# Kernel optimization log

Hardware: AMD Instinct MI355X
Metric: run time of the kernel (lower is better)

The kernel has to match this reference:

```python
import jax, jax.numpy as jnp
import numpy as np

B, N, C, D = 64, 1024, 128, 64

def setup_inputs() -> dict:
    key = jax.random.key(0)
    ks = jax.random.split(key, 7)
    # kaiming_normal_ on weights (fan_in = C), default zero-ish biases kept as Linear default uniform; use small uniform
    std = float(np.sqrt(2.0 / C))
    bb = float(1.0 / np.sqrt(C))
    return {
        "x": jax.random.normal(ks[0], (B, N, C), jnp.float32),
        "Wq": jax.random.normal(ks[1], (C, D), jnp.float32) * std,
        "bq": jax.random.uniform(ks[2], (D,), jnp.float32, -bb, bb),
        "Wk": jax.random.normal(ks[3], (C, D), jnp.float32) * std,
        "bk": jax.random.uniform(ks[4], (D,), jnp.float32, -bb, bb),
        "Wv": jax.random.normal(ks[5], (C, D), jnp.float32) * std,
        "bv": jax.random.uniform(ks[6], (D,), jnp.float32, -bb, bb),
    }

def reference(x, Wq, bq, Wk, bk, Wv, bv):
    q = jax.nn.relu(jnp.einsum('bnc,cd->bnd', x, Wq) + bq)  # [B,N,D]
    k = jax.nn.relu(jnp.einsum('bnc,cd->bnd', x, Wk) + bk)
    v = jax.nn.relu(jnp.einsum('bnc,cd->bnd', x, Wv) + bv)
    scores = jnp.einsum('bnd,bmd->bnm', q, k) / jnp.sqrt(jnp.asarray(D, q.dtype))
    attn = jax.nn.softmax(scores, axis=-1)
    out = jnp.einsum('bnm,bmd->bnd', attn, v)
    return out + q
```

## Files before the change

### kernel.cpp

```cpp
#include <hip/hip_runtime.h>
#include <hip/hip_bf16.h>


#define Bsz 64
#define Nsz 1024
#define Csz 128
#define Dsz 64

typedef __attribute__((ext_vector_type(8))) short short8;
typedef __attribute__((ext_vector_type(4))) float f32x4;

__device__ __forceinline__ unsigned short f2bf(float f) {
    union { float f; unsigned u; } v; v.f = f;
    unsigned r = v.u + 0x7FFF + ((v.u >> 16) & 1);
    return (unsigned short)(r >> 16);
}
__device__ __forceinline__ float bf2f(unsigned short h) {
    union { unsigned u; float f; } v; v.u = ((unsigned)h) << 16;
    return v.f;
}
__device__ __forceinline__ unsigned pack_bf16rn(float lo, float hi) {
    unsigned ulo = __float_as_uint(lo) + 0x8000u;
    unsigned uhi = __float_as_uint(hi) + 0x8000u;
    return __builtin_amdgcn_perm(uhi, ulo, 0x07060302u);
}

#define SCq (0.125f * 1.44269504f)
#define INV_SC (1.0f / (0.125f * 1.44269504f))

__global__ __launch_bounds__(256) void wprep_kernel(
    const float* __restrict__ Wq, const float* __restrict__ Wk,
    const float* __restrict__ Wv, unsigned short* __restrict__ wfrag)
{
    int t = blockIdx.x * 256 + threadIdx.x;
    int lane = t & 63, ksi = (t >> 6) & 3, dt = t >> 8;
    int l16 = lane & 15, quad = lane >> 4;
    int d = dt * 16 + l16;
    int c0 = ksi * 32 + quad * 8;
    short8 h8, l8, k8, v8;
    #pragma unroll
    for (int j = 0; j < 8; j++) {
        float w = Wq[(c0 + j) * Dsz + d];
        unsigned short h = f2bf(w);
        h8[j] = (short)h;
        l8[j] = (short)f2bf(w - bf2f(h));
        k8[j] = (short)f2bf(Wk[(c0 + j) * Dsz + d]);
        v8[j] = (short)f2bf(Wv[(c0 + j) * Dsz + d]);
    }
    int idx = (dt * 4 + ksi) * 64 + lane;
    ((short8*)wfrag)[0 * 1024 + idx] = h8;
    ((short8*)wfrag)[1 * 1024 + idx] = l8;
    ((short8*)wfrag)[2 * 1024 + idx] = k8;
    ((short8*)wfrag)[3 * 1024 + idx] = v8;
}

__global__ __launch_bounds__(256) void qkv_kernel(
    const float* __restrict__ x, const unsigned short* __restrict__ wfrag,
    const float* __restrict__ bq, const float* __restrict__ bk,
    const float* __restrict__ bv,
    unsigned short* __restrict__ qs, unsigned short* __restrict__ ks2,
    unsigned short* __restrict__ vt2)
{
    __shared__ short xh[8192];
    __shared__ short xl[8192];
    const int t    = threadIdx.x;
    const int lane = t & 63;
    const int l16  = lane & 15, quad = lane >> 4;
    const int dt   = t >> 6;
    const long rowbase = (long)blockIdx.x * 64;
    const int d = dt * 16 + l16;

    short8 wqh[4], wql[4], wkf[4], wvf[4];
    #pragma unroll
    for (int ksi = 0; ksi < 4; ksi++) {
        int idx = (dt * 4 + ksi) * 64 + lane;
        wqh[ksi] = ((const short8*)wfrag)[0 * 1024 + idx];
        wql[ksi] = ((const short8*)wfrag)[1 * 1024 + idx];
        wkf[ksi] = ((const short8*)wfrag)[2 * 1024 + idx];
        wvf[ksi] = ((const short8*)wfrag)[3 * 1024 + idx];
    }

    {
        const int row = t & 63;
        const float* xrow = x + (rowbase + row) * Csz;
        #pragma unroll
        for (int p = 0; p < 4; p++) {
            int cb = (t >> 6) + p * 4;
            float4 a = *(const float4*)(xrow + cb * 8);
            float4 bb = *(const float4*)(xrow + cb * 8 + 4);
            float f[8] = {a.x, a.y, a.z, a.w, bb.x, bb.y, bb.z, bb.w};
            short8 hi, lo;
            #pragma unroll
            for (int i = 0; i < 8; i++) {
                unsigned short h = f2bf(f[i]);
                hi[i] = (short)h;
                lo[i] = (short)f2bf(f[i] - bf2f(h));
            }
            int unit = ((row >> 4) * 4 + (cb >> 2)) * 64 + ((row & 15) | ((cb & 3) << 4));
            *(short8*)&xh[unit * 8] = hi;
            *(short8*)&xl[unit * 8] = lo;
        }
    }
    __syncthreads();

    f32x4 aq[4], ak[4], av[4];
    #pragma unroll
    for (int i = 0; i < 4; i++) {
        aq[i] = (f32x4){0.f, 0.f, 0.f, 0.f};
        ak[i] = (f32x4){0.f, 0.f, 0.f, 0.f};
        av[i] = (f32x4){0.f, 0.f, 0.f, 0.f};
    }
    #pragma unroll
    for (int ksi = 0; ksi < 4; ksi++) {
        #pragma unroll
        for (int rt = 0; rt < 4; rt++) {
            short8 ah = *(const short8*)&xh[((rt * 4 + ksi) * 64 + lane) * 8];
            short8 al = *(const short8*)&xl[((rt * 4 + ksi) * 64 + lane) * 8];
            aq[rt] = __builtin_amdgcn_mfma_f32_16x16x32_bf16(ah, wqh[ksi], aq[rt], 0, 0, 0);
            aq[rt] = __builtin_amdgcn_mfma_f32_16x16x32_bf16(al, wqh[ksi], aq[rt], 0, 0, 0);
            aq[rt] = __builtin_amdgcn_mfma_f32_16x16x32_bf16(ah, wql[ksi], aq[rt], 0, 0, 0);
            ak[rt] = __builtin_amdgcn_mfma_f32_16x16x32_bf16(ah, wkf[ksi], ak[rt], 0, 0, 0);
            av[rt] = __builtin_amdgcn_mfma_f32_16x16x32_bf16(ah, wvf[ksi], av[rt], 0, 0, 0);
        }
    }

    const float bqd = bq[d], bkd = bk[d], bvd = bv[d];
    const long b  = rowbase >> 10;
    const int  kt = (int)((rowbase >> 6) & 15);

    const int half  = dt >> 1;
    const int quadk = ((dt & 1) << 1) | (l16 >> 3);
    const int jk    = l16 & 7;
    unsigned short* kbase = ks2 + ((((long)(b * 16 + kt) * 4) * 2 + half) * 64) * 8;

    float vv[4][4];
    #pragma unroll
    for (int rt = 0; rt < 4; rt++) {
        #pragma unroll
        for (int r = 0; r < 4; r++) {
            long n = rowbase + rt * 16 + quad * 4 + r;
            float q = fmaxf(aq[rt][r] + bqd, 0.f);
            float k = fmaxf(ak[rt][r] + bkd, 0.f);
            vv[r][rt] = fmaxf(av[rt][r] + bvd, 0.f);
            qs[n * Dsz + d] = f2bf(q * SCq);
            kbase[((long)rt * 2 * 64 + quadk * 16 + quad * 4 + r) * 8 + jk] = f2bf(k);
        }
    }
    const int ck = quad >> 1;
    const int quadp = (quad & 1) * 2;
    long vidx = (((long)(b * 16 + kt) * 4 + dt) * 2 + ck) * 64 + quadp * 16 + l16;
    uint4 o0 = make_uint4(pack_bf16rn(vv[0][0], vv[0][1]), pack_bf16rn(vv[0][2], vv[0][3]),
                          pack_bf16rn(vv[1][0], vv[1][1]), pack_bf16rn(vv[1][2], vv[1][3]));
    uint4 o1 = make_uint4(pack_bf16rn(vv[2][0], vv[2][1]), pack_bf16rn(vv[2][2], vv[2][3]),
                          pack_bf16rn(vv[3][0], vv[3][1]), pack_bf16rn(vv[3][2], vv[3][3]));
    ((uint4*)vt2)[vidx]      = o0;
    ((uint4*)vt2)[vidx + 16] = o1;
}

__global__ __launch_bounds__(256) void attn_kernel(
    const unsigned short* __restrict__ qs,
    const unsigned short* __restrict__ ks2,
    const unsigned short* __restrict__ vt2,
    float* __restrict__ out)
{
    __shared__ short Pl[4][32][72];

    const int t    = threadIdx.x;
    const int wave = t >> 6;
    const int lane = t & 63;
    const int l16  = lane & 15;
    const int quad = lane >> 4;
    const int b    = blockIdx.x & 63;
    const int qh   = blockIdx.x >> 6;
    const int qbase = qh * 128 + wave * 32;

    const short8* ks8 = (const short8*)ks2 + (long)b * (16 * 4 * 2 * 64);
    const short8* vt8 = (const short8*)vt2 + (long)b * (16 * 4 * 2 * 64);

    short8 aq[2][2];
    #pragma unroll
    for (int s = 0; s < 2; s++) {
        const unsigned short* qp = qs + ((long)b * Nsz + qbase + s * 16 + l16) * Dsz + quad * 8;
        aq[s][0] = *(const short8*)(qp);
        aq[s][1] = *(const short8*)(qp + 32);
    }

    f32x4 O[2][4];
    float lsum[2][4];
    #pragma unroll
    for (int s = 0; s < 2; s++)
        #pragma unroll
        for (int i = 0; i < 4; i++) { O[s][i] = (f32x4){0.f,0.f,0.f,0.f}; lsum[s][i] = 0.f; }

    short8 kf[4][2];
    #pragma unroll
    for (int kb = 0; kb < 4; kb++) {
        kf[kb][0] = ks8[(kb * 2 + 0) * 64 + lane];
        kf[kb][1] = ks8[(kb * 2 + 1) * 64 + lane];
    }

    for (int kt = 0; kt < 16; kt++) {
        short8 bvf[2][4];
        #pragma unroll
        for (int cb = 0; cb < 4; cb++) {
            bvf[0][cb] = vt8[((long)kt * 8 + cb * 2 + 0) * 64 + lane];
            bvf[1][cb] = vt8[((long)kt * 8 + cb * 2 + 1) * 64 + lane];
        }

        f32x4 sc[2][4];
        #pragma unroll
        for (int s = 0; s < 2; s++) {
            #pragma unroll
            for (int kb = 0; kb < 4; kb++) {
                f32x4 z = (f32x4){0.f, 0.f, 0.f, 0.f};
                z = __builtin_amdgcn_mfma_f32_16x16x32_bf16(aq[s][0], kf[kb][0], z, 0, 0, 0);
                z = __builtin_amdgcn_mfma_f32_16x16x32_bf16(aq[s][1], kf[kb][1], z, 0, 0, 0);
                sc[s][kb] = z;
            }
        }

        short8 kf2[4][2];
        {
            int ktn = (kt + 1) & 15;
            #pragma unroll
            for (int kb = 0; kb < 4; kb++) {
                kf2[kb][0] = ks8[((long)ktn * 8 + kb * 2 + 0) * 64 + lane];
                kf2[kb][1] = ks8[((long)ktn * 8 + kb * 2 + 1) * 64 + lane];
            }
        }

        #pragma unroll
        for (int s = 0; s < 2; s++) {
            #pragma unroll
            for (int r = 0; r < 4; r++) {
                float p0 = __builtin_amdgcn_exp2f(sc[s][0][r]);
                float p1 = __builtin_amdgcn_exp2f(sc[s][1][r]);
                float p2 = __builtin_amdgcn_exp2f(sc[s][2][r]);
                float p3 = __builtin_amdgcn_exp2f(sc[s][3][r]);
                lsum[s][r] += (p0 + p1) + (p2 + p3);
                *(uint2*)&Pl[wave][s * 16 + quad * 4 + r][l16 * 4] =
                    make_uint2(pack_bf16rn(p0, p1), pack_bf16rn(p2, p3));
            }
        }

        #pragma unroll
        for (int ck = 0; ck < 2; ck++) {
            #pragma unroll
            for (int s = 0; s < 2; s++) {
                short8 ap = *(const short8*)&Pl[wave][s * 16 + l16][ck * 32 + quad * 8];
                #pragma unroll
                for (int cb = 0; cb < 4; cb++) {
                    O[s][cb] = __builtin_amdgcn_mfma_f32_16x16x32_bf16(ap, bvf[ck][cb], O[s][cb], 0, 0, 0);
                }
            }
        }

        #pragma unroll
        for (int kb = 0; kb < 4; kb++) { kf[kb][0] = kf2[kb][0]; kf[kb][1] = kf2[kb][1]; }
    }

    #pragma unroll
    for (int s = 0; s < 2; s++)
        #pragma unroll
        for (int r = 0; r < 4; r++)
            #pragma unroll
            for (int off = 1; off < 16; off <<= 1)
                lsum[s][r] += __shfl_xor(lsum[s][r], off);

    #pragma unroll
    for (int s = 0; s < 2; s++) {
        #pragma unroll
        for (int r = 0; r < 4; r++) {
            float rl = 1.0f / lsum[s][r];
            long nrow = (long)b * Nsz + qbase + s * 16 + quad * 4 + r;
            #pragma unroll
            for (int cb = 0; cb < 4; cb++) {
                int d = cb * 16 + l16;
                float qv = bf2f(qs[nrow * Dsz + d]) * INV_SC;
                out[nrow * Dsz + d] = O[s][cb][r] * rl + qv;
            }
        }
    }
}

extern "C" void kernel_launch(void* const* d_in, const int* in_sizes, int n_in,
                              void* d_out, int out_size, void* d_ws, size_t ws_size,
                              hipStream_t stream) {
    const float* x  = (const float*)d_in[0];
    const float* Wq = (const float*)d_in[1];
    const float* bq = (const float*)d_in[2];
    const float* Wk = (const float*)d_in[3];
    const float* bk = (const float*)d_in[4];
    const float* Wv = (const float*)d_in[5];
    const float* bv = (const float*)d_in[6];
    float* out = (float*)d_out;

    char* ws = (char*)d_ws;
    unsigned short* qsc   = (unsigned short*)ws;
    unsigned short* ks2   = (unsigned short*)(ws + 0x1000000);
    unsigned short* vt2   = (unsigned short*)(ws + 0x2000000);
    unsigned short* wfrag = (unsigned short*)(ws + 0x3000000);

    wprep_kernel<<<dim3(4), dim3(256), 0, stream>>>(Wq, Wk, Wv, wfrag);
    qkv_kernel<<<dim3(1024), dim3(256), 0, stream>>>(
        x, wfrag, bq, bk, bv, qsc, ks2, vt2);
    attn_kernel<<<dim3(512), dim3(256), 0, stream>>>(
        qsc, ks2, vt2, out);
}
```

Before: 120.7 us.

## Fuse QKV projection into attention kernel, recomputing K/V per block in LDS

Merges the projection and attention kernels into one launch. Each block computes its own Q tile into shared memory and recomputes K and V for every key tile of its batch on the fly. This removes the global write and re-read of the bf16 Q/K/V intermediates and one launch. In exchange, the K/V projection work and x reads are duplicated across the 8 query blocks of each batch, and extra block-wide barriers are added per key tile.

```diff
diff --git a/kernel.cpp b/kernel.cpp
--- a/kernel.cpp
+++ b/kernel.cpp
@@ -54,21 +54,25 @@
     ((short8*)wfrag)[3 * 1024 + idx] = v8;
 }
 
-__global__ __launch_bounds__(256) void qkv_kernel(
+__global__ __launch_bounds__(256, 2) void fused_kernel(
     const float* __restrict__ x, const unsigned short* __restrict__ wfrag,
     const float* __restrict__ bq, const float* __restrict__ bk,
-    const float* __restrict__ bv,
-    unsigned short* __restrict__ qs, unsigned short* __restrict__ ks2,
-    unsigned short* __restrict__ vt2)
+    const float* __restrict__ bv, float* __restrict__ out)
 {
-    __shared__ short xh[8192];
-    __shared__ short xl[8192];
+    __shared__ short Xs[8192];
+    __shared__ short KVb[2][4096];
+    __shared__ short Qs[128][72];
+    __shared__ short Pl[4][32][72];
+
     const int t    = threadIdx.x;
     const int lane = t & 63;
-    const int l16  = lane & 15, quad = lane >> 4;
-    const int dt   = t >> 6;
-    const long rowbase = (long)blockIdx.x * 64;
-    const int d = dt * 16 + l16;
+    const int l16  = lane & 15;
+    const int quad = lane >> 4;
+    const int wave = t >> 6;
+    const int dt   = wave;
+    const int b    = blockIdx.x & 63;
+    const int qh   = blockIdx.x >> 6;
+    const int d    = dt * 16 + l16;
 
     short8 wqh[4], wql[4], wkf[4], wvf[4];
     #pragma unroll
@@ -79,134 +83,138 @@
         wkf[ksi] = ((const short8*)wfrag)[2 * 1024 + idx];
         wvf[ksi] = ((const short8*)wfrag)[3 * 1024 + idx];
     }
-
-    {
-        const int row = t & 63;
-        const float* xrow = x + (rowbase + row) * Csz;
-        #pragma unroll
-        for (int p = 0; p < 4; p++) {
-            int cb = (t >> 6) + p * 4;
-            float4 a = *(const float4*)(xrow + cb * 8);
-            float4 bb = *(const float4*)(xrow + cb * 8 + 4);
-            float f[8] = {a.x, a.y, a.z, a.w, bb.x, bb.y, bb.z, bb.w};
-            short8 hi, lo;
-            #pragma unroll
-            for (int i = 0; i < 8; i++) {
-                unsigned short h = f2bf(f[i]);
-                hi[i] = (short)h;
-                lo[i] = (short)f2bf(f[i] - bf2f(h));
-            }
-            int unit = ((row >> 4) * 4 + (cb >> 2)) * 64 + ((row & 15) | ((cb & 3) << 4));
-            *(short8*)&xh[unit * 8] = hi;
-            *(short8*)&xl[unit * 8] = lo;
-        }
-    }
-    __syncthreads();
-
-    f32x4 aq[4], ak[4], av[4];
-    #pragma unroll
-    for (int i = 0; i < 4; i++) {
-        aq[i] = (f32x4){0.f, 0.f, 0.f, 0.f};
-        ak[i] = (f32x4){0.f, 0.f, 0.f, 0.f};
-        av[i] = (f32x4){0.f, 0.f, 0.f, 0.f};
-    }
-    #pragma unroll
-    for (int ksi = 0; ksi < 4; ksi++) {
-        #pragma unroll
-        for (int rt = 0; rt < 4; rt++) {
-            short8 ah = *(const short8*)&xh[((rt * 4 + ksi) * 64 + lane) * 8];
-            short8 al = *(const short8*)&xl[((rt * 4 + ksi) * 64 + lane) * 8];
-            aq[rt] = __builtin_amdgcn_mfma_f32_16x16x32_bf16(ah, wqh[ksi], aq[rt], 0, 0, 0);
-            aq[rt] = __builtin_amdgcn_mfma_f32_16x16x32_bf16(al, wqh[ksi], aq[rt], 0, 0, 0);
-            aq[rt] = __builtin_amdgcn_mfma_f32_16x16x32_bf16(ah, wql[ksi], aq[rt], 0, 0, 0);
-            ak[rt] = __builtin_amdgcn_mfma_f32_16x16x32_bf16(ah, wkf[ksi], ak[rt], 0, 0, 0);
-            av[rt] = __builtin_amdgcn_mfma_f32_16x16x32_bf16(ah, wvf[ksi], av[rt], 0, 0, 0);
-        }
-    }
-
     const float bqd = bq[d], bkd = bk[d], bvd = bv[d];
-    const long b  = rowbase >> 10;
-    const int  kt = (int)((rowbase >> 6) & 15);
+
+    #pragma unroll 1
+    for (int h64 = 0; h64 < 2; h64++) {
+        const long rowbase = (long)b * Nsz + qh * 128 + h64 * 64;
+        {
+            const int row = t & 63;
+            const float* xrow = x + (rowbase + row) * Csz;
+            short* xl = &KVb[0][0];
+            #pragma unroll
+            for (int p = 0; p < 4; p++) {
+                int cb = (t >> 6) + p * 4;
+                float4 a  = *(const float4*)(xrow + cb * 8);
+                float4 b2 = *(const float4*)(xrow + cb * 8 + 4);
+                float f[8] = {a.x, a.y, a.z, a.w, b2.x, b2.y, b2.z, b2.w};
+                short8 hi, lo;
+                #pragma unroll
+                for (int i = 0; i < 8; i++) {
+                    unsigned short h = f2bf(f[i]);
+                    hi[i] = (short)h;
+                    lo[i] = (short)f2bf(f[i] - bf2f(h));
+                }
+                int unit = ((row >> 4) * 4 + (cb >> 2)) * 64 + ((row & 15) | ((cb & 3) << 4));
+                *(short8*)&Xs[unit * 8] = hi;
+                *(short8*)&xl[unit * 8] = lo;
+            }
+        }
+        __syncthreads();
+        f32x4 aqc[4];
+        #pragma unroll
+        for (int i = 0; i < 4; i++) aqc[i] = (f32x4){0.f, 0.f, 0.f, 0.f};
+        #pragma unroll
+        for (int ksi = 0; ksi < 4; ksi++) {
+            #pragma unroll
+            for (int rt = 0; rt < 4; rt++) {
+                short8 ah = *(const short8*)&Xs[((rt * 4 + ksi) * 64 + lane) * 8];
+                short8 al = *(const short8*)&KVb[0][((rt * 4 + ksi) * 64 + lane) * 8];
+                aqc[rt] = __builtin_amdgcn_mfma_f32_16x16x32_bf16(ah, wqh[ksi], aqc[rt], 0, 0, 0);
+                aqc[rt] = __builtin_amdgcn_mfma_f32_16x16x32_bf16(al, wqh[ksi], aqc[rt], 0, 0, 0);
+                aqc[rt] = __builtin_amdgcn_mfma_f32_16x16x32_bf16(ah, wql[ksi], aqc[rt], 0, 0, 0);
+            }
+        }
+        #pragma unroll
+        for (int rt = 0; rt < 4; rt++)
+            #pragma unroll
+            for (int r = 0; r < 4; r++) {
+                float q = fmaxf(aqc[rt][r] + bqd, 0.f);
+                Qs[h64 * 64 + rt * 16 + quad * 4 + r][d] = f2bf(q * SCq);
+            }
+        __syncthreads();
+    }
+
+    short8 aq[2][2];
+    #pragma unroll
+    for (int s = 0; s < 2; s++) {
+        aq[s][0] = *(const short8*)&Qs[wave * 32 + s * 16 + l16][quad * 8];
+        aq[s][1] = *(const short8*)&Qs[wave * 32 + s * 16 + l16][32 + quad * 8];
+    }
+
+    f32x4 O[2][4];
+    float lsum[2][4];
+    #pragma unroll
+    for (int s = 0; s < 2; s++)
+        #pragma unroll
+        for (int i = 0; i < 4; i++) { O[s][i] = (f32x4){0.f,0.f,0.f,0.f}; lsum[s][i] = 0.f; }
 
     const int half  = dt >> 1;
     const int quadk = ((dt & 1) << 1) | (l16 >> 3);
     const int jk    = l16 & 7;
-    unsigned short* kbase = ks2 + ((((long)(b * 16 + kt) * 4) * 2 + half) * 64) * 8;
-
-    float vv[4][4];
-    #pragma unroll
-    for (int rt = 0; rt < 4; rt++) {
-        #pragma unroll
-        for (int r = 0; r < 4; r++) {
-            long n = rowbase + rt * 16 + quad * 4 + r;
-            float q = fmaxf(aq[rt][r] + bqd, 0.f);
-            float k = fmaxf(ak[rt][r] + bkd, 0.f);
-            vv[r][rt] = fmaxf(av[rt][r] + bvd, 0.f);
-            qs[n * Dsz + d] = f2bf(q * SCq);
-            kbase[((long)rt * 2 * 64 + quadk * 16 + quad * 4 + r) * 8 + jk] = f2bf(k);
-        }
-    }
-    const int ck = quad >> 1;
+    const int ckk   = quad >> 1;
     const int quadp = (quad & 1) * 2;
-    long vidx = (((long)(b * 16 + kt) * 4 + dt) * 2 + ck) * 64 + quadp * 16 + l16;
-    uint4 o0 = make_uint4(pack_bf16rn(vv[0][0], vv[0][1]), pack_bf16rn(vv[0][2], vv[0][3]),
-                          pack_bf16rn(vv[1][0], vv[1][1]), pack_bf16rn(vv[1][2], vv[1][3]));
-    uint4 o1 = make_uint4(pack_bf16rn(vv[2][0], vv[2][1]), pack_bf16rn(vv[2][2], vv[2][3]),
-                          pack_bf16rn(vv[3][0], vv[3][1]), pack_bf16rn(vv[3][2], vv[3][3]));
-    ((uint4*)vt2)[vidx]      = o0;
-    ((uint4*)vt2)[vidx + 16] = o1;
-}
-
-__global__ __launch_bounds__(256) void attn_kernel(
-    const unsigned short* __restrict__ qs,
-    const unsigned short* __restrict__ ks2,
-    const unsigned short* __restrict__ vt2,
-    float* __restrict__ out)
-{
-    __shared__ short Pl[4][32][72];
-
-    const int t    = threadIdx.x;
-    const int wave = t >> 6;
-    const int lane = t & 63;
-    const int l16  = lane & 15;
-    const int quad = lane >> 4;
-    const int b    = blockIdx.x & 63;
-    const int qh   = blockIdx.x >> 6;
-    const int qbase = qh * 128 + wave * 32;
-
-    const short8* ks8 = (const short8*)ks2 + (long)b * (16 * 4 * 2 * 64);
-    const short8* vt8 = (const short8*)vt2 + (long)b * (16 * 4 * 2 * 64);
-
-    short8 aq[2][2];
-    #pragma unroll
-    for (int s = 0; s < 2; s++) {
-        const unsigned short* qp = qs + ((long)b * Nsz + qbase + s * 16 + l16) * Dsz + quad * 8;
-        aq[s][0] = *(const short8*)(qp);
-        aq[s][1] = *(const short8*)(qp + 32);
-    }
-
-    f32x4 O[2][4];
-    float lsum[2][4];
-    #pragma unroll
-    for (int s = 0; s < 2; s++)
-        #pragma unroll
-        for (int i = 0; i < 4; i++) { O[s][i] = (f32x4){0.f,0.f,0.f,0.f}; lsum[s][i] = 0.f; }
-
-    short8 kf[4][2];
-    #pragma unroll
-    for (int kb = 0; kb < 4; kb++) {
-        kf[kb][0] = ks8[(kb * 2 + 0) * 64 + lane];
-        kf[kb][1] = ks8[(kb * 2 + 1) * 64 + lane];
-    }
-
+
+    #pragma unroll 1
     for (int kt = 0; kt < 16; kt++) {
-        short8 bvf[2][4];
-        #pragma unroll
-        for (int cb = 0; cb < 4; cb++) {
-            bvf[0][cb] = vt8[((long)kt * 8 + cb * 2 + 0) * 64 + lane];
-            bvf[1][cb] = vt8[((long)kt * 8 + cb * 2 + 1) * 64 + lane];
-        }
-
+        {
+            const long rowbase = (long)b * Nsz + kt * 64;
+            const int row = t & 63;
+            const float* xrow = x + (rowbase + row) * Csz;
+            #pragma unroll
+            for (int p = 0; p < 4; p++) {
+                int cb = (t >> 6) + p * 4;
+                float4 a  = *(const float4*)(xrow + cb * 8);
+                float4 b2 = *(const float4*)(xrow + cb * 8 + 4);
+                float f[8] = {a.x, a.y, a.z, a.w, b2.x, b2.y, b2.z, b2.w};
+                short8 hi;
+                #pragma unroll
+                for (int i = 0; i < 8; i++) hi[i] = (short)f2bf(f[i]);
+                int unit = ((row >> 4) * 4 + (cb >> 2)) * 64 + ((row & 15) | ((cb & 3) << 4));
+                *(short8*)&Xs[unit * 8] = hi;
+            }
+        }
+        __syncthreads();
+
+        f32x4 ak[4], av[4];
+        #pragma unroll
+        for (int i = 0; i < 4; i++) {
+            ak[i] = (f32x4){0.f, 0.f, 0.f, 0.f};
+            av[i] = (f32x4){0.f, 0.f, 0.f, 0.f};
+        }
+        #pragma unroll
+        for (int ksi = 0; ksi < 4; ksi++) {
+            #pragma unroll
+            for (int rt = 0; rt < 4; rt++) {
+                short8 ah = *(const short8*)&Xs[((rt * 4 + ksi) * 64 + lane) * 8];
+                ak[rt] = __builtin_amdgcn_mfma_f32_16x16x32_bf16(ah, wkf[ksi], ak[rt], 0, 0, 0);
+                av[rt] = __builtin_amdgcn_mfma_f32_16x16x32_bf16(ah, wvf[ksi], av[rt], 0, 0, 0);
+            }
+        }
+        float vv[4][4];
+        #pragma unroll
+        for (int rt = 0; rt < 4; rt++) {
+            #pragma unroll
+            for (int r = 0; r < 4; r++) {
+                float kv = fmaxf(ak[rt][r] + bkd, 0.f);
+                vv[r][rt] = fmaxf(av[rt][r] + bvd, 0.f);
+                KVb[0][(rt * 2 + half) * 512 + (quadk * 16 + quad * 4 + r) * 8 + jk] = f2bf(kv);
+            }
+        }
+        uint4 o0 = make_uint4(pack_bf16rn(vv[0][0], vv[0][1]), pack_bf16rn(vv[0][2], vv[0][3]),
+                              pack_bf16rn(vv[1][0], vv[1][1]), pack_bf16rn(vv[1][2], vv[1][3]));
+        uint4 o1 = make_uint4(pack_bf16rn(vv[2][0], vv[2][1]), pack_bf16rn(vv[2][2], vv[2][3]),
+                              pack_bf16rn(vv[3][0], vv[3][1]), pack_bf16rn(vv[3][2], vv[3][3]));
+        *(uint4*)&KVb[1][(dt * 2 + ckk) * 512 + (quadp * 16 + l16) * 8]      = o0;
+        *(uint4*)&KVb[1][(dt * 2 + ckk) * 512 + (quadp * 16 + 16 + l16) * 8] = o1;
+        __syncthreads();
+
+        short8 kf[4][2];
+        #pragma unroll
+        for (int kb = 0; kb < 4; kb++) {
+            kf[kb][0] = *(const short8*)&KVb[0][(kb * 2 + 0) * 512 + lane * 8];
+            kf[kb][1] = *(const short8*)&KVb[0][(kb * 2 + 1) * 512 + lane * 8];
+        }
         f32x4 sc[2][4];
         #pragma unroll
         for (int s = 0; s < 2; s++) {
@@ -218,17 +226,12 @@
                 sc[s][kb] = z;
             }
         }
-
-        short8 kf2[4][2];
-        {
-            int ktn = (kt + 1) & 15;
-            #pragma unroll
-            for (int kb = 0; kb < 4; kb++) {
-                kf2[kb][0] = ks8[((long)ktn * 8 + kb * 2 + 0) * 64 + lane];
-                kf2[kb][1] = ks8[((long)ktn * 8 + kb * 2 + 1) * 64 + lane];
-            }
-        }
-
+        short8 bvf[2][4];
+        #pragma unroll
+        for (int cb = 0; cb < 4; cb++) {
+            bvf[0][cb] = *(const short8*)&KVb[1][(cb * 2 + 0) * 512 + lane * 8];
+            bvf[1][cb] = *(const short8*)&KVb[1][(cb * 2 + 1) * 512 + lane * 8];
+        }
         #pragma unroll
         for (int s = 0; s < 2; s++) {
             #pragma unroll
@@ -242,7 +245,6 @@
                     make_uint2(pack_bf16rn(p0, p1), pack_bf16rn(p2, p3));
             }
         }
-
         #pragma unroll
         for (int ck = 0; ck < 2; ck++) {
             #pragma unroll
@@ -254,9 +256,7 @@
                 }
             }
         }
-
-        #pragma unroll
-        for (int kb = 0; kb < 4; kb++) { kf[kb][0] = kf2[kb][0]; kf[kb][1] = kf2[kb][1]; }
+        __syncthreads();
     }
 
     #pragma unroll
@@ -272,12 +272,13 @@
         #pragma unroll
         for (int r = 0; r < 4; r++) {
             float rl = 1.0f / lsum[s][r];
-            long nrow = (long)b * Nsz + qbase + s * 16 + quad * 4 + r;
+            int lrow = wave * 32 + s * 16 + quad * 4 + r;
+            long nrow = (long)b * Nsz + qh * 128 + lrow;
             #pragma unroll
             for (int cb = 0; cb < 4; cb++) {
-                int d = cb * 16 + l16;
-                float qv = bf2f(qs[nrow * Dsz + d]) * INV_SC;
-                out[nrow * Dsz + d] = O[s][cb][r] * rl + qv;
+                int d2 = cb * 16 + l16;
+                float qv = bf2f((unsigned short)Qs[lrow][d2]) * INV_SC;
+                out[nrow * Dsz + d2] = O[s][cb][r] * rl + qv;
             }
         }
     }
@@ -295,15 +296,9 @@
     const float* bv = (const float*)d_in[6];
     float* out = (float*)d_out;
 
-    char* ws = (char*)d_ws;
-    unsigned short* qsc   = (unsigned short*)ws;
-    unsigned short* ks2   = (unsigned short*)(ws + 0x1000000);
-    unsigned short* vt2   = (unsigned short*)(ws + 0x2000000);
-    unsigned short* wfrag = (unsigned short*)(ws + 0x3000000);
+    unsigned short* wfrag = (unsigned short*)d_ws;
 
     wprep_kernel<<<dim3(4), dim3(256), 0, stream>>>(Wq, Wk, Wv, wfrag);
-    qkv_kernel<<<dim3(1024), dim3(256), 0, stream>>>(
-        x, wfrag, bq, bk, bv, qsc, ks2, vt2);
-    attn_kernel<<<dim3(512), dim3(256), 0, stream>>>(
-        qsc, ks2, vt2, out);
-}
+    fused_kernel<<<dim3(512), dim3(256), 0, stream>>>(
+        x, wfrag, bq, bk, bv, out);
+}
```

Result: slower. 149.4 us (+23.8%).
